# Kernel tuning notes

Hardware: AMD Instinct MI355X
Metric: run time of the kernel (lower is better)

Reference implementation:

```python
import jax, jax.numpy as jnp
import numpy as np

N_NODES = 100000
HIDDEN = 64
IN_CH = 128
N_EDGES = 1600000


def setup_inputs() -> dict:
    key = jax.random.key(0)
    ks = jax.random.split(key, 12)
    x = jax.random.normal(ks[0], (N_NODES, IN_CH), dtype=jnp.float32)
    edge_index = jax.random.randint(ks[1], (2, N_EDGES), 0, N_NODES, dtype=jnp.int64)

    def glorot(k, fan_in, fan_out):
        s = jnp.sqrt(6.0 / (fan_in + fan_out)).astype(jnp.float32)
        return jax.random.uniform(k, (fan_in, fan_out), jnp.float32, -s, s)

    return {
        "x": x,
        "edge_index": edge_index,
        # GCNConv layer 1: linear (no bias) + post-aggregation bias
        "W1": glorot(ks[2], IN_CH, HIDDEN),
        "b1": jnp.zeros((HIDDEN,), jnp.float32),
        # GCNConv layer 2
        "W2": glorot(ks[3], HIDDEN, HIDDEN),
        "b2": jnp.zeros((HIDDEN,), jnp.float32),
        # edge classifier MLP: Linear(2H,H) -> ReLU -> Linear(H,2)
        "Wc1": glorot(ks[4], 2 * HIDDEN, HIDDEN),
        "bc1": jnp.zeros((HIDDEN,), jnp.float32),
        "Wc2": glorot(ks[5], HIDDEN, 2),
        "bc2": jnp.zeros((2,), jnp.float32),
    }


def _gcn_forward(x, edge_index, W1, b1, W2, b2, Wc1, bc1, Wc2, bc2):
    n = x.shape[0]
    src, dst = edge_index[0], edge_index[1]
    # add self-loops (PyG GCNConv default)
    loop = jnp.arange(n, dtype=edge_index.dtype)
    a_src = jnp.concatenate([src, loop])  # [E+N]
    a_dst = jnp.concatenate([dst, loop])
    # symmetric normalization: deg over destination with unit edge weights
    deg = jax.ops.segment_sum(jnp.ones(a_dst.shape[0], x.dtype), a_dst, num_segments=n)
    dis = jax.lax.rsqrt(deg)  # deg >= 1 due to self-loops
    norm = dis[a_src] * dis[a_dst]  # [E+N]

    def conv(h, W, b):
        h = h @ W  # [N, H]
        msg = h[a_src] * norm[:, None]  # [E+N, H] gather + scale
        return jax.ops.segment_sum(msg, a_dst, num_segments=n) + b

    h = jax.nn.relu(conv(x, W1, b1))  # dropout is identity in eval mode
    h = conv(h, W2, b2)
    # edge classifier on concatenated endpoint embeddings
    e = jnp.concatenate([h[src], h[dst]], axis=1)  # [E, 2H]
    z = jax.nn.relu(e @ Wc1 + bc1)
    return z @ Wc2 + bc2  # [E, 2]


def reference(x, edge_index, W1, b1, W2, b2, Wc1, bc1, Wc2, bc2):
    return _gcn_forward(x, edge_index, W1, b1, W2, b2, Wc1, bc1, Wc2, bc2)
```

## Files before the change

kernel.cpp:

```cpp
#include <hip/hip_runtime.h>
#include <hip/hip_fp16.h>

#define HID 64
#define BKT_SHIFT 10
#define BKT_NODES 1024
#define PCHUNKS 512

typedef _Float16 half8 __attribute__((ext_vector_type(8)));
typedef _Float16 half4 __attribute__((ext_vector_type(4)));
typedef float f32x4 __attribute__((ext_vector_type(4)));

__global__ __launch_bounds__(256) void k_bkt_count(const int* __restrict__ dst,
                                                   int* __restrict__ G, int E,
                                                   int nbkt, int chunk) {
  __shared__ int hist[128];
  int p = blockIdx.x, tid = threadIdx.x;
  for (int i = tid; i < nbkt; i += 256) hist[i] = 0;
  __syncthreads();
  int s = p * chunk, e = min(s + chunk, E);
  for (int i = s + tid; i < e; i += 256) atomicAdd(&hist[dst[i] >> BKT_SHIFT], 1);
  __syncthreads();
  for (int b = tid; b < nbkt; b += 256) G[b * PCHUNKS + p] = hist[b];
}

__global__ void k_scan1(const int* __restrict__ in, int* __restrict__ scanout,
                        int* __restrict__ blocksums, int n) {
  __shared__ int sdata[256];
  int tid = threadIdx.x;
  int base = blockIdx.x * 1024 + tid * 4;
  int v0 = 0, v1 = 0, v2 = 0, v3 = 0;
  if (base + 0 < n) v0 = in[base + 0];
  if (base + 1 < n) v1 = in[base + 1];
  if (base + 2 < n) v2 = in[base + 2];
  if (base + 3 < n) v3 = in[base + 3];
  int tsum = v0 + v1 + v2 + v3;
  sdata[tid] = tsum;
  __syncthreads();
  for (int off = 1; off < 256; off <<= 1) {
    int t = (tid >= off) ? sdata[tid - off] : 0;
    __syncthreads();
    sdata[tid] += t;
    __syncthreads();
  }
  int excl = sdata[tid] - tsum;
  if (base + 0 < n) scanout[base + 0] = excl;
  if (base + 1 < n) scanout[base + 1] = excl + v0;
  if (base + 2 < n) scanout[base + 2] = excl + v0 + v1;
  if (base + 3 < n) scanout[base + 3] = excl + v0 + v1 + v2;
  if (tid == 255) blocksums[blockIdx.x] = sdata[255];
}

__global__ void k_scan2(int* blocksums, int nb) {
  __shared__ int s[128];
  int tid = threadIdx.x;
  int v = (tid < nb) ? blocksums[tid] : 0;
  s[tid] = v;
  __syncthreads();
  for (int off = 1; off < 128; off <<= 1) {
    int t = (tid >= off) ? s[tid - off] : 0;
    __syncthreads();
    s[tid] += t;
    __syncthreads();
  }
  if (tid < nb) blocksums[tid] = s[tid] - v;
}

__global__ void k_scan3(const int* __restrict__ scanout,
                        const int* __restrict__ blocksums, int* __restrict__ outp,
                        int n) {
  int i = blockIdx.x * blockDim.x + threadIdx.x;
  if (i < n) outp[i] = scanout[i] + blocksums[i >> 10];
}

__global__ __launch_bounds__(256) void k_bkt_scatter(
    const int* __restrict__ src, const int* __restrict__ dst,
    const int* __restrict__ Gscan, int* __restrict__ psrc,
    unsigned short* __restrict__ pdst, int E, int nbkt, int chunk) {
  __shared__ int gbase[128];
  __shared__ int rcnt[128];
  int p = blockIdx.x, tid = threadIdx.x;
  for (int b = tid; b < nbkt; b += 256) {
    gbase[b] = Gscan[b * PCHUNKS + p];
    rcnt[b] = 0;
  }
  __syncthreads();
  int s = p * chunk, e = min(s + chunk, E);
  for (int i = s + tid; i < e; i += 256) {
    int d = dst[i];
    int b = d >> BKT_SHIFT;
    int r = atomicAdd(&rcnt[b], 1);
    int pos = gbase[b] + r;
    psrc[pos] = src[i];
    pdst[pos] = (unsigned short)(d & (BKT_NODES - 1));
  }
}

__global__ __launch_bounds__(1024) void k_bkt_final(
    const int* __restrict__ Gscan, const int* __restrict__ psrc,
    const unsigned short* __restrict__ pdst, int* __restrict__ rowoff,
    float* __restrict__ dis, int* __restrict__ csr_src, int E, int nbkt, int N) {
  __shared__ int cnt[BKT_NODES];
  __shared__ int lo[BKT_NODES];
  int b = blockIdx.x, tid = threadIdx.x;
  int s = Gscan[b * PCHUNKS];
  int eend = (b + 1 < nbkt) ? Gscan[(b + 1) * PCHUNKS] : E;
  cnt[tid] = 0;
  __syncthreads();
  for (int i = s + tid; i < eend; i += 1024) atomicAdd(&cnt[pdst[i]], 1);
  __syncthreads();
  int v = cnt[tid];
  lo[tid] = v;
  __syncthreads();
  for (int off = 1; off < 1024; off <<= 1) {
    int t = (tid >= off) ? lo[tid - off] : 0;
    __syncthreads();
    lo[tid] += t;
    __syncthreads();
  }
  int excl = lo[tid] - v;
  int node = b * BKT_NODES + tid;
  if (node < N) {
    rowoff[node] = s + excl;
    dis[node] = rsqrtf((float)v + 1.0f);
  }
  __syncthreads();
  lo[tid] = excl;
  cnt[tid] = 0;
  __syncthreads();
  for (int i = s + tid; i < eend; i += 1024) {
    int ln = pdst[i];
    int r = atomicAdd(&cnt[ln], 1);
    csr_src[s + lo[ln] + r] = psrc[i];
  }
}

__global__ void k_pack_all(const float* __restrict__ W1, const float* __restrict__ W2,
                           const float* __restrict__ Wc1, const float* __restrict__ bc1,
                           __half* __restrict__ packW1, __half* __restrict__ packW2,
                           __half* __restrict__ packUV, float* __restrict__ biasUV,
                           __half* __restrict__ ysent) {
  int b = blockIdx.x, tid = threadIdx.x;
  if (b < 4) {
    int t = b * 256 + tid;
    int f = t >> 6, L = t & 63;
    int kc = f >> 2, nb = f & 3;
    int k = 32 * kc + ((L >> 4) << 3);
    int n = (L & 15) + 16 * nb;
    for (int j = 0; j < 8; ++j)
      packW1[(t << 3) + j] = __float2half(W1[(k + j) * 64 + n]);
  } else if (b < 6) {
    int t = (b - 4) * 256 + tid;
    int f = t >> 6, L = t & 63;
    int kc = f >> 2, nb = f & 3;
    int k = 32 * kc + ((L >> 4) << 3);
    int n = (L & 15) + 16 * nb;
    for (int j = 0; j < 8; ++j)
      packW2[(t << 3) + j] = __float2half(W2[(k + j) * 64 + n]);
  } else if (b < 10) {
    int t = (b - 6) * 256 + tid;
    int f = t >> 6, L = t & 63;
    int kc = f >> 3, nb = f & 7;
    int k = 32 * kc + ((L >> 4) << 3);
    int n = (L & 15) + 16 * nb;
    for (int j = 0; j < 8; ++j) {
      float w = (n < 64) ? Wc1[(k + j) * 64 + n] : Wc1[(64 + k + j) * 64 + (n - 64)];
      packUV[(t << 3) + j] = __float2half(w);
    }
  } else {
    if (tid < 128) biasUV[tid] = (tid < 64) ? bc1[tid] : 0.f;
    else if (tid < 192) ysent[tid - 128] = __float2half(0.f);
  }
}

template <int K, int NOUT, bool F32IN>
__global__ __launch_bounds__(256) void k_lin_mfma(
    const void* __restrict__ Xv, const __half* __restrict__ packB,
    const float* __restrict__ bias, const float* __restrict__ dis,
    __half* __restrict__ Y, int n) {
  int wid = blockIdx.x * 4 + (threadIdx.x >> 6);
  int rowbase = wid * 16;
  if (rowbase >= n) return;
  int L = threadIdx.x & 63;
  int m16 = L & 15, quad = L >> 4;
  constexpr int KC = K / 32;
  constexpr int NB = NOUT / 16;

  half8 Bf[KC * NB];
  const half8* packv = (const half8*)packB;
#pragma unroll
  for (int f = 0; f < KC * NB; ++f) Bf[f] = packv[f * 64 + L];

  int r = min(rowbase + m16, n - 1);
  half8 Af[KC];
  if (F32IN) {
    const float* xr = (const float*)Xv + (long)r * K;
#pragma unroll
    for (int kc = 0; kc < KC; ++kc) {
      const float4* xp = (const float4*)(xr + kc * 32 + quad * 8);
      float4 a = xp[0], b = xp[1];
      half8 v = {(_Float16)a.x, (_Float16)a.y, (_Float16)a.z, (_Float16)a.w,
                 (_Float16)b.x, (_Float16)b.y, (_Float16)b.z, (_Float16)b.w};
      Af[kc] = v;
    }
  } else {
    const half8* xr = (const half8*)((const __half*)Xv + (long)r * K);
#pragma unroll
    for (int kc = 0; kc < KC; ++kc) Af[kc] = xr[kc * 4 + quad];
  }

  f32x4 acc[NB];
#pragma unroll
  for (int nb = 0; nb < NB; ++nb) acc[nb] = {0.f, 0.f, 0.f, 0.f};
#pragma unroll
  for (int kc = 0; kc < KC; ++kc)
#pragma unroll
    for (int nb = 0; nb < NB; ++nb)
      acc[nb] = __builtin_amdgcn_mfma_f32_16x16x32_f16(Af[kc], Bf[kc * NB + nb],
                                                       acc[nb], 0, 0, 0);

  float dv[4];
#pragma unroll
  for (int j = 0; j < 4; ++j) {
    int ro = rowbase + quad * 4 + j;
    dv[j] = (dis && ro < n) ? dis[ro] : 1.f;
  }
#pragma unroll
  for (int nb = 0; nb < NB; ++nb) {
    int col = m16 + 16 * nb;
    float bv = bias ? bias[col] : 0.f;
#pragma unroll
    for (int j = 0; j < 4; ++j) {
      int ro = rowbase + quad * 4 + j;
      if (ro < n) {
        float v = (acc[nb][j] + bv) * dv[j];
        Y[(long)ro * NOUT + col] = __float2half(v);
      }
    }
  }
}

__global__ __launch_bounds__(256) void k_agg_csr(
    const __half* __restrict__ Yh, const float* __restrict__ dis,
    const int* __restrict__ rowoff, const int* __restrict__ csr_src,
    const float* __restrict__ b, __half* __restrict__ A, int n, int E, int relu) {
  int node = blockIdx.x * 4 + (threadIdx.x >> 6);
  if (node >= n) return;
  int L = threadIdx.x & 63;
  int sub = L >> 4;
  int cq = L & 15;
  const half4* Y4 = (const half4*)Yh;
  float dd = dis[node];
  int i0 = rowoff[node];
  int end = (node == n - 1) ? E : rowoff[node + 1];

  float z[4][4] = {{0.f}};
  if (sub == 0) {
    half4 hv = Y4[(long)node * 16 + cq];
#pragma unroll
    for (int j = 0; j < 4; ++j) z[0][j] = (float)hv[j];
  }

  int last = end - 1;
  for (int base = i0; base < end; base += 16) {
    int sidx[4];
#pragma unroll
    for (int slot = 0; slot < 4; ++slot) {
      int idx = base + slot * 4 + sub;
      int sl = csr_src[min(idx, last)];
      sidx[slot] = (idx < end) ? sl : n;
    }
#pragma unroll
    for (int slot = 0; slot < 4; ++slot) {
      half4 hv = Y4[(long)sidx[slot] * 16 + cq];
#pragma unroll
      for (int j = 0; j < 4; ++j) z[slot][j] += (float)hv[j];
    }
  }

  float a[4];
#pragma unroll
  for (int j = 0; j < 4; ++j) {
    a[j] = (z[0][j] + z[1][j]) + (z[2][j] + z[3][j]);
    a[j] += __shfl_xor(a[j], 16, 64);
    a[j] += __shfl_xor(a[j], 32, 64);
  }
  if (sub == 0) {
    float4 bb = ((const float4*)b)[cq];
    float v0 = fmaf(a[0], dd, bb.x), v1 = fmaf(a[1], dd, bb.y);
    float v2 = fmaf(a[2], dd, bb.z), v3 = fmaf(a[3], dd, bb.w);
    if (relu) {
      v0 = fmaxf(v0, 0.f); v1 = fmaxf(v1, 0.f);
      v2 = fmaxf(v2, 0.f); v3 = fmaxf(v3, 0.f);
    }
    half4 o = {(_Float16)v0, (_Float16)v1, (_Float16)v2, (_Float16)v3};
    ((half4*)A)[(long)node * 16 + cq] = o;
  }
}

__global__ __launch_bounds__(256) void k_edge_mlp(
    const __half* __restrict__ UV, const int* __restrict__ src,
    const int* __restrict__ dst, const float* __restrict__ Wc2,
    const float* __restrict__ bc2, float* __restrict__ out, int E, int nwaves) {
  int wid = blockIdx.x * 4 + (threadIdx.x >> 6);
  int L = threadIdx.x & 63;
  int sub = L >> 4;
  int cq = L & 15;

  float w0[4], w1[4];
#pragma unroll
  for (int j = 0; j < 4; ++j) {
    int c = cq * 4 + j;
    w0[j] = Wc2[2 * c];
    w1[j] = Wc2[2 * c + 1];
  }
  float ob0 = bc2[0], ob1 = bc2[1];

  const half4* UV4 = (const half4*)UV;
  int last = E - 1;

  for (long base = (long)wid * 32; base < E; base += (long)nwaves * 32) {
    int se[8], de[8];
#pragma unroll
    for (int slot = 0; slot < 8; ++slot) {
      int e = (int)base + slot * 4 + sub;
      int ec = min(e, last);
      se[slot] = src[ec];
      de[slot] = dst[ec];
    }
    half4 uu[8], vv[8];
#pragma unroll
    for (int slot = 0; slot < 8; ++slot) {
      uu[slot] = UV4[(long)se[slot] * 32 + cq];
      vv[slot] = UV4[(long)de[slot] * 32 + 16 + cq];
    }
#pragma unroll
    for (int slot = 0; slot < 8; ++slot) {
      float o0 = 0.f, o1 = 0.f;
#pragma unroll
      for (int j = 0; j < 4; ++j) {
        float v = fmaxf((float)uu[slot][j] + (float)vv[slot][j], 0.f);
        o0 = fmaf(v, w0[j], o0);
        o1 = fmaf(v, w1[j], o1);
      }
      o0 += __shfl_xor(o0, 1, 64);
      o1 += __shfl_xor(o1, 1, 64);
      o0 += __shfl_xor(o0, 2, 64);
      o1 += __shfl_xor(o1, 2, 64);
      o0 += __shfl_xor(o0, 4, 64);
      o1 += __shfl_xor(o1, 4, 64);
      o0 += __shfl_xor(o0, 8, 64);
      o1 += __shfl_xor(o1, 8, 64);
      int e = (int)base + slot * 4 + sub;
      if (cq == 0 && e < E) {
        float2 o = {o0 + ob0, o1 + ob1};
        *(float2*)(out + 2 * (long)e) = o;
      }
    }
  }
}

extern "C" void kernel_launch(void* const* d_in, const int* in_sizes, int n_in,
                              void* d_out, int out_size, void* d_ws, size_t ws_size,
                              hipStream_t stream) {
  const float* x   = (const float*)d_in[0];
  const int*   ei  = (const int*)d_in[1];
  const float* W1  = (const float*)d_in[2];
  const float* b1  = (const float*)d_in[3];
  const float* W2  = (const float*)d_in[4];
  const float* b2  = (const float*)d_in[5];
  const float* Wc1 = (const float*)d_in[6];
  const float* bc1 = (const float*)d_in[7];
  const float* Wc2 = (const float*)d_in[8];
  const float* bc2 = (const float*)d_in[9];

  const int N = in_sizes[0] / 128;
  const int E = in_sizes[1] / 2;
  const int* src = ei;
  const int* dst = ei + E;

  const int nbkt = (N + BKT_NODES - 1) >> BKT_SHIFT;
  const int gsz = nbkt * PCHUNKS;
  const int chunk = (E + PCHUNKS - 1) / PCHUNKS;

  float* dis     = (float*)d_ws;
  __half* y      = (__half*)(dis + N);
  __half* h      = y + (long)(N + 1) * HID;
  __half* UV     = h + (long)N * HID;
  __half* packW1 = UV + (long)N * 128;
  __half* packW2 = packW1 + 8192;
  __half* packUV = packW2 + 4096;
  float* biasUV  = (float*)(packUV + 8192);
  int* rowoff    = (int*)(biasUV + 128);
  int* csr_src   = rowoff + N;
  int* G         = csr_src + E;
  int* Gs1       = G + gsz;
  int* Gbs       = Gs1 + gsz;
  int* Gscan     = Gbs + 128;
  int* psrc            = (int*)UV;
  unsigned short* pdst = (unsigned short*)(psrc + E);

  const int B = 256;
  int nbScan = (gsz + 1023) / 1024;

  k_pack_all<<<11, B, 0, stream>>>(W1, W2, Wc1, bc1, packW1, packW2, packUV,
                                   biasUV, y + (long)N * HID);
  k_bkt_count<<<PCHUNKS, B, 0, stream>>>(dst, G, E, nbkt, chunk);
  k_scan1<<<nbScan, B, 0, stream>>>(G, Gs1, Gbs, gsz);
  k_scan2<<<1, 128, 0, stream>>>(Gbs, nbScan);
  k_scan3<<<(gsz + B - 1) / B, B, 0, stream>>>(Gs1, Gbs, Gscan, gsz);
  k_bkt_scatter<<<PCHUNKS, B, 0, stream>>>(src, dst, Gscan, psrc, pdst, E, nbkt,
                                           chunk);
  k_bkt_final<<<nbkt, 1024, 0, stream>>>(Gscan, psrc, pdst, rowoff, dis, csr_src,
                                         E, nbkt, N);

  int gAgg = (N + 3) / 4;
  int gLin = (N + 63) / 64;

  k_lin_mfma<128, 64, true><<<gLin, B, 0, stream>>>(x, packW1, nullptr, dis, y, N);
  k_agg_csr<<<gAgg, B, 0, stream>>>(y, dis, rowoff, csr_src, b1, h, N, E, 1);

  k_lin_mfma<64, 64, false><<<gLin, B, 0, stream>>>(h, packW2, nullptr, dis, y, N);
  k_agg_csr<<<gAgg, B, 0, stream>>>(y, dis, rowoff, csr_src, b2, h, N, E, 0);

  k_lin_mfma<64, 128, false><<<gLin, B, 0, stream>>>(h, packUV, biasUV, nullptr, UV, N);
  int cblocks = 2048;
  int nwaves = cblocks * 4;
  k_edge_mlp<<<cblocks, B, 0, stream>>>(UV, src, dst, Wc2, bc2,
                                        (float*)d_out, E, nwaves);
}
```

Baseline: 343.0 us.

## Process edge classifier in CSR (dst-sorted) order with scattered output writes

The bucket sort now records each edge's original index and writes per-edge dst and eid arrays in CSR order. The edge MLP then walks edges sorted by destination, so V-row gathers hit the cache better, and writes each result to its original edge slot. This adds extra index writes and reads in the sort kernels and turns the output stores into scattered writes.

Result: slower. 388.5 us (+13.3%).

```diff
diff --git a/kernel.cpp b/kernel.cpp
--- a/kernel.cpp
+++ b/kernel.cpp
@@ -75,7 +75,8 @@
 __global__ __launch_bounds__(256) void k_bkt_scatter(
     const int* __restrict__ src, const int* __restrict__ dst,
     const int* __restrict__ Gscan, int* __restrict__ psrc,
-    unsigned short* __restrict__ pdst, int E, int nbkt, int chunk) {
+    unsigned short* __restrict__ pdst, int* __restrict__ peid, int E, int nbkt,
+    int chunk) {
   __shared__ int gbase[128];
   __shared__ int rcnt[128];
   int p = blockIdx.x, tid = threadIdx.x;
@@ -92,13 +93,15 @@
     int pos = gbase[b] + r;
     psrc[pos] = src[i];
     pdst[pos] = (unsigned short)(d & (BKT_NODES - 1));
+    peid[pos] = i;
   }
 }
 
 __global__ __launch_bounds__(1024) void k_bkt_final(
     const int* __restrict__ Gscan, const int* __restrict__ psrc,
-    const unsigned short* __restrict__ pdst, int* __restrict__ rowoff,
-    float* __restrict__ dis, int* __restrict__ csr_src, int E, int nbkt, int N) {
+    const unsigned short* __restrict__ pdst, const int* __restrict__ peid,
+    int* __restrict__ rowoff, float* __restrict__ dis, int* __restrict__ csr_src,
+    int* __restrict__ csr_dst, int* __restrict__ csr_eid, int E, int nbkt, int N) {
   __shared__ int cnt[BKT_NODES];
   __shared__ int lo[BKT_NODES];
   int b = blockIdx.x, tid = threadIdx.x;
@@ -130,7 +133,10 @@
   for (int i = s + tid; i < eend; i += 1024) {
     int ln = pdst[i];
     int r = atomicAdd(&cnt[ln], 1);
-    csr_src[s + lo[ln] + r] = psrc[i];
+    int pos = s + lo[ln] + r;
+    csr_src[pos] = psrc[i];
+    csr_dst[pos] = b * BKT_NODES + ln;
+    csr_eid[pos] = peid[i];
   }
 }
 
@@ -297,10 +303,11 @@
   }
 }
 
-__global__ __launch_bounds__(256) void k_edge_mlp(
-    const __half* __restrict__ UV, const int* __restrict__ src,
-    const int* __restrict__ dst, const float* __restrict__ Wc2,
-    const float* __restrict__ bc2, float* __restrict__ out, int E, int nwaves) {
+__global__ __launch_bounds__(256) void k_edge_mlp_csr(
+    const __half* __restrict__ UV, const int* __restrict__ csr_src,
+    const int* __restrict__ csr_dst, const int* __restrict__ csr_eid,
+    const float* __restrict__ Wc2, const float* __restrict__ bc2,
+    float* __restrict__ out, int E, int nwaves) {
   int wid = blockIdx.x * 4 + (threadIdx.x >> 6);
   int L = threadIdx.x & 63;
   int sub = L >> 4;
@@ -319,13 +326,14 @@
   int last = E - 1;
 
   for (long base = (long)wid * 32; base < E; base += (long)nwaves * 32) {
-    int se[8], de[8];
+    int se[8], de[8], eid[8];
 #pragma unroll
     for (int slot = 0; slot < 8; ++slot) {
       int e = (int)base + slot * 4 + sub;
       int ec = min(e, last);
-      se[slot] = src[ec];
-      de[slot] = dst[ec];
+      se[slot] = csr_src[ec];
+      de[slot] = csr_dst[ec];
+      eid[slot] = csr_eid[ec];
     }
     half4 uu[8], vv[8];
 #pragma unroll
@@ -353,7 +361,7 @@
       int e = (int)base + slot * 4 + sub;
       if (cq == 0 && e < E) {
         float2 o = {o0 + ob0, o1 + ob1};
-        *(float2*)(out + 2 * (long)e) = o;
+        *(float2*)(out + 2 * (long)eid[slot]) = o;
       }
     }
   }
@@ -392,12 +400,15 @@
   float* biasUV  = (float*)(packUV + 8192);
   int* rowoff    = (int*)(biasUV + 128);
   int* csr_src   = rowoff + N;
-  int* G         = csr_src + E;
+  int* csr_dst   = csr_src + E;
+  int* csr_eid   = csr_dst + E;
+  int* G         = csr_eid + E;
   int* Gs1       = G + gsz;
   int* Gbs       = Gs1 + gsz;
   int* Gscan     = Gbs + 128;
   int* psrc            = (int*)UV;
   unsigned short* pdst = (unsigned short*)(psrc + E);
+  int* peid            = (int*)(pdst + E);
 
   const int B = 256;
   int nbScan = (gsz + 1023) / 1024;
@@ -408,10 +419,10 @@
   k_scan1<<<nbScan, B, 0, stream>>>(G, Gs1, Gbs, gsz);
   k_scan2<<<1, 128, 0, stream>>>(Gbs, nbScan);
   k_scan3<<<(gsz + B - 1) / B, B, 0, stream>>>(Gs1, Gbs, Gscan, gsz);
-  k_bkt_scatter<<<PCHUNKS, B, 0, stream>>>(src, dst, Gscan, psrc, pdst, E, nbkt,
-                                           chunk);
-  k_bkt_final<<<nbkt, 1024, 0, stream>>>(Gscan, psrc, pdst, rowoff, dis, csr_src,
-                                         E, nbkt, N);
+  k_bkt_scatter<<<PCHUNKS, B, 0, stream>>>(src, dst, Gscan, psrc, pdst, peid, E,
+                                           nbkt, chunk);
+  k_bkt_final<<<nbkt, 1024, 0, stream>>>(Gscan, psrc, pdst, peid, rowoff, dis,
+                                         csr_src, csr_dst, csr_eid, E, nbkt, N);
 
   int gAgg = (N + 3) / 4;
   int gLin = (N + 63) / 64;
@@ -425,6 +436,6 @@
   k_lin_mfma<64, 128, false><<<gLin, B, 0, stream>>>(h, packUV, biasUV, nullptr, UV, N);
   int cblocks = 2048;
   int nwaves = cblocks * 4;
-  k_edge_mlp<<<cblocks, B, 0, stream>>>(UV, src, dst, Wc2, bc2,
-                                        (float*)d_out, E, nwaves);
-}
+  k_edge_mlp_csr<<<cblocks, B, 0, stream>>>(UV, csr_src, csr_dst, csr_eid, Wc2,
+                                            bc2, (float*)d_out, E, nwaves);
+}
```
